# Optimization experiments

Measured on AMD Instinct MI355X. Metric: run time of the kernel, lower is better.

## Reference

```python
import jax, jax.numpy as jnp
import numpy as np

B, L, D, H = 2, 4096, 768, 12
HS = D // H  # head_size = 64
SCALE = HS ** -0.5


def setup_inputs() -> dict:
    key = jax.random.key(0)
    k1, k2, k3 = jax.random.split(key, 3)
    x = jax.random.normal(k1, (B, L, D), dtype=jnp.float32)
    # torch nn.Linear weights are [out_features, in_features]; y = x @ W.T
    Wq = jax.random.normal(k2, (D, D), dtype=jnp.float32) * (D ** -0.5)
    Wo = jax.random.normal(k3, (D, D), dtype=jnp.float32) * (D ** -0.5)
    return {"x": x, "Wq": Wq, "Wo": Wo}


def reference(x, Wq, Wo):
    b, l, d = x.shape
    # NOTE: source module uses self.query for Q, K, AND V (bug preserved).
    q = jnp.einsum('bld,ed->ble', x, Wq)              # [B,L,D]
    q = q.reshape(b, l, H, HS).transpose(0, 2, 1, 3)   # [B,H,L,HS]
    k = v = q                                          # K = V = Q (faithful)
    scores = jnp.einsum('bhqd,bhkd->bhqk', q, k) * SCALE  # [B,H,L,L]
    attn = jax.nn.softmax(scores, axis=-1)
    out = jnp.einsum('bhqk,bhkd->bhqd', attn, v)       # [B,H,L,HS]
    out = out.transpose(0, 2, 1, 3).reshape(b, l, d)   # [B,L,D]
    out = jnp.einsum('bld,ed->ble', out, Wo)           # output projection
    return out
```

## Files before the change

### kernel.cpp

```cpp
#include <hip/hip_runtime.h>
#include <hip/hip_bf16.h>

#define LQ 4096
#define DQ 768
#define NH 12
#define NB 2

typedef __attribute__((ext_vector_type(8))) short short8;
typedef __attribute__((ext_vector_type(2))) unsigned uint2v;
typedef __attribute__((ext_vector_type(4))) float f32x4;

__device__ __forceinline__ short f2bf(float f) {
    union { float f; unsigned u; } v; v.f = f;
    unsigned r = v.u + 0x7FFFu + ((v.u >> 16) & 1u);
    return (short)(r >> 16);
}

__device__ __forceinline__ unsigned pk2(float a, float b) {
    float2 t; t.x = a; t.y = b;
    __hip_bfloat162 h = __float22bfloat162_rn(t);
    unsigned u; __builtin_memcpy(&u, &h, 4);
    return u;
}

__device__ __forceinline__ f32x4 mfma16(short8 a, short8 b, f32x4 c) {
    return __builtin_amdgcn_mfma_f32_16x16x32_bf16(a, b, c, 0, 0, 0);
}

__device__ __forceinline__ void gld16(const short* g, short* l) {
    __builtin_amdgcn_global_load_lds(
        (const __attribute__((address_space(1))) unsigned int*)(g),
        (__attribute__((address_space(3))) unsigned int*)(l), 16, 0, 0);
}

#define SQRT_C 0.424660891f

__global__ __launch_bounds__(256) void cvtw(const float* __restrict__ a,
                                            short* __restrict__ o) {
    int i = blockIdx.x * 256 + threadIdx.x;
    float4 v = ((const float4*)a)[i];
    *(uint2v*)&o[i * 4] = (uint2v){pk2(v.x, v.y), pk2(v.z, v.w)};
}


template <int MODE>
__global__ __launch_bounds__(256, 3) void gemm_nt(const short* __restrict__ A,
                                                  const short* __restrict__ Wb,
                                                  void* __restrict__ Cp,
                                                  short* __restrict__ Vf) {
    __shared__ __attribute__((aligned(16))) short As[2][128 * 64];
    __shared__ __attribute__((aligned(16))) short Bs[2][64 * 64];
    const int t = threadIdx.x;
    const int lane = t & 63, w = t >> 6;
    const int lr = lane & 15, qd = lane >> 4;
    const int wm = (w & 1) * 64, wn = (w >> 1) * 32;
    const int lin = blockIdx.x;
    const int xcd = lin & 7, jj = lin >> 3;
    const int nt = jj % 12, mt = (jj / 12) * 8 + xcd;
    const int m0 = mt * 128, n0 = nt * 64;

    int aoffs[4], boffs[2];
#pragma unroll
    for (int u = 0; u < 4; ++u) {
        int c = (u * 4 + w) * 64 + lane;
        int row = c >> 3, k = (c & 7) ^ (row & 7);
        aoffs[u] = (m0 + row) * DQ + k * 8;
    }
#pragma unroll
    for (int u = 0; u < 2; ++u) {
        int c = (u * 4 + w) * 64 + lane;
        int row = c >> 3, k = (c & 7) ^ (row & 7);
        boffs[u] = (n0 + row) * DQ + k * 8;
    }

    f32x4 acc[4][2];
#pragma unroll
    for (int i = 0; i < 4; ++i)
#pragma unroll
        for (int j = 0; j < 2; ++j) acc[i][j] = (f32x4){0.f, 0.f, 0.f, 0.f};

#pragma unroll
    for (int u = 0; u < 4; ++u) gld16(&A[aoffs[u]], &As[0][(u * 4 + w) * 512]);
#pragma unroll
    for (int u = 0; u < 2; ++u) gld16(&Wb[boffs[u]], &Bs[0][(u * 4 + w) * 512]);
    __syncthreads();

    int cur = 0;
    for (int kt = 0; kt < 12; ++kt) {
        if (kt < 11) {
            const int k0 = (kt + 1) * 64;
#pragma unroll
            for (int u = 0; u < 4; ++u) gld16(&A[aoffs[u] + k0], &As[cur ^ 1][(u * 4 + w) * 512]);
#pragma unroll
            for (int u = 0; u < 2; ++u) gld16(&Wb[boffs[u] + k0], &Bs[cur ^ 1][(u * 4 + w) * 512]);
        }
#pragma unroll
        for (int s = 0; s < 2; ++s) {
            const int cq = ((4 * s + qd) ^ (lr & 7)) * 8;
            short8 af[4], bf[2];
#pragma unroll
            for (int i = 0; i < 4; ++i)
                af[i] = *(short8*)&As[cur][(wm + 16 * i + lr) * 64 + cq];
#pragma unroll
            for (int j = 0; j < 2; ++j)
                bf[j] = *(short8*)&Bs[cur][(wn + 16 * j + lr) * 64 + cq];
#pragma unroll
            for (int i = 0; i < 4; ++i)
#pragma unroll
                for (int j = 0; j < 2; ++j)
                    acc[i][j] = mfma16(af[i], bf[j], acc[i][j]);
        }
        __syncthreads();
        cur ^= 1;
    }

    if (MODE == 0) {
#pragma unroll
        for (int i = 0; i < 4; ++i)
#pragma unroll
            for (int j = 0; j < 2; ++j) {
                const int row0 = m0 + wm + 16 * i + qd * 4;
                const int col = n0 + wn + 16 * j + lr;
#pragma unroll
                for (int r = 0; r < 4; ++r)
                    ((float*)Cp)[(size_t)(row0 + r) * DQ + col] = acc[i][j][r];
            }
    } else {
        short* Qf = (short*)Cp;
        short* F = (short*)As;
        const int bh = (m0 >> 12) * NH + nt;
        const size_t gbase = (size_t)bh * (LQ * 64) + (size_t)(((m0 & 4095) >> 6) << 12);
#pragma unroll
        for (int i = 0; i < 4; ++i)
#pragma unroll
            for (int j = 0; j < 2; ++j) {
                const int kl = wm + 16 * i + qd * 4;
                const int hs = wn + 16 * j + lr;
                const int fi = ((kl >> 6) << 12) + ((((hs >> 4) << 1) + ((kl >> 5) & 1)) << 9)
                             + (((hs & 15) + (((kl >> 3) & 3) << 4)) << 3) + (kl & 7);
                *(uint2v*)&F[fi] = (uint2v){pk2(acc[i][j][0], acc[i][j][1]),
                                            pk2(acc[i][j][2], acc[i][j][3])};
            }
        __syncthreads();
#pragma unroll
        for (int p = 0; p < 4; ++p) {
            int u = t + 256 * p;
            *(short8*)&Vf[gbase + (size_t)u * 8] = *(short8*)&F[u * 8];
        }
        __syncthreads();
#pragma unroll
        for (int i = 0; i < 4; ++i)
#pragma unroll
            for (int j = 0; j < 2; ++j) {
                const int hs = wn + 16 * j + lr;
#pragma unroll
                for (int r = 0; r < 4; ++r) {
                    const int key = wm + 16 * i + qd * 4 + r;
                    const int fi = ((key >> 6) << 12) + (((((key >> 4) & 3) << 1) + (hs >> 5)) << 9)
                                 + (((qd * 4 + r) + (((hs >> 3) & 3) << 4)) << 3) + (hs & 7);
                    F[fi] = f2bf(acc[i][j][r] * SQRT_C);
                }
            }
        __syncthreads();
#pragma unroll
        for (int p = 0; p < 4; ++p) {
            int u = t + 256 * p;
            *(short8*)&Qf[gbase + (size_t)u * 8] = *(short8*)&F[u * 8];
        }
    }
}

__global__ __launch_bounds__(256, 3) void attn(const short* __restrict__ Qf,
                                               const short* __restrict__ Vf,
                                               short* __restrict__ O) {
    const int linear = blockIdx.x;
    const int xcd = linear & 7, slot = linear >> 3;
    const int bh = 3 * xcd + (slot >> 5);
    const int qtile = slot & 31;
    const int t = threadIdx.x;
    const int lane = t & 63, w = t >> 6;
    const int qw = w & 1, half = w >> 1;
    const int lr = lane & 15, qd = lane >> 4;

    __shared__ alignas(16) char smem[43008];
    short* aqs = (short*)smem;
    short* Ps = (short*)(smem + 16384) + w * 2560;

    const short* Qbh = Qf + (size_t)bh * (LQ * 64);
    const short* Vbh = Vf + (size_t)bh * (LQ * 64);
    const int q0 = qtile * 128 + qw * 64;
    const int kb0 = half * 64;

    const short one_bf = (short)0x3F80;
    short8 ones;
#pragma unroll
    for (int j = 0; j < 8; ++j) ones[j] = one_bf;

#pragma unroll
    for (int p = 0; p < 4; ++p) {
        int off = (t + 256 * p) * 8;
        *(short8*)&aqs[off] = *(const short8*)&Qbh[(size_t)qtile * 8192 + off];
    }
    __syncthreads();

    f32x4 oacc[4][4], lacc[4];
#pragma unroll
    for (int i = 0; i < 4; ++i) {
        lacc[i] = (f32x4){0.f, 0.f, 0.f, 0.f};
#pragma unroll
        for (int t2 = 0; t2 < 4; ++t2) oacc[i][t2] = (f32x4){0.f, 0.f, 0.f, 0.f};
    }

    const int aqbase = qw * 4096 + lane * 8;

    for (int kb = kb0; kb < kb0 + 64; ++kb) {
        short8 kf[2][2];
#pragma unroll
        for (int t4 = 0; t4 < 2; ++t4)
#pragma unroll
            for (int s = 0; s < 2; ++s)
                kf[t4][s] = *(const short8*)&Qbh[kb * 2048 + (t4 * 2 + s) * 512 + lane * 8];

#pragma unroll
        for (int i = 0; i < 4; ++i) {
            short8 aq0 = *(const short8*)&aqs[aqbase + i * 1024];
            short8 aq1 = *(const short8*)&aqs[aqbase + i * 1024 + 512];
            f32x4 s0 = (f32x4){0.f, 0.f, 0.f, 0.f};
            f32x4 s1 = (f32x4){0.f, 0.f, 0.f, 0.f};
            s0 = mfma16(kf[0][0], aq0, s0);
            s0 = mfma16(kf[0][1], aq1, s0);
            s1 = mfma16(kf[1][0], aq0, s1);
            s1 = mfma16(kf[1][1], aq1, s1);
            *(uint2v*)&Ps[i * 640 + lr * 40 + 4 * qd] =
                (uint2v){pk2(__builtin_amdgcn_exp2f(s0[0]), __builtin_amdgcn_exp2f(s0[1])),
                         pk2(__builtin_amdgcn_exp2f(s0[2]), __builtin_amdgcn_exp2f(s0[3]))};
            *(uint2v*)&Ps[i * 640 + lr * 40 + 16 + 4 * qd] =
                (uint2v){pk2(__builtin_amdgcn_exp2f(s1[0]), __builtin_amdgcn_exp2f(s1[1])),
                         pk2(__builtin_amdgcn_exp2f(s1[2]), __builtin_amdgcn_exp2f(s1[3]))};
        }

        short8 vb[4];
#pragma unroll
        for (int t2 = 0; t2 < 4; ++t2)
            vb[t2] = *(const short8*)&Vbh[(kb >> 1) * 4096 + (kb & 1) * 512 + t2 * 1024 + lane * 8];

#pragma unroll
        for (int i = 0; i < 4; ++i) {
            short8 pa = *(short8*)&Ps[i * 640 + lr * 40 + qd * 8];
#pragma unroll
            for (int t2 = 0; t2 < 4; ++t2)
                oacc[i][t2] = mfma16(pa, vb[t2], oacc[i][t2]);
            lacc[i] = mfma16(pa, ones, lacc[i]);
        }
    }

    __syncthreads();
    f32x4* ex = (f32x4*)smem + (qw * 64 + lane) * 21;
    if (half) {
#pragma unroll
        for (int i = 0; i < 4; ++i) {
#pragma unroll
            for (int t2 = 0; t2 < 4; ++t2) ex[i * 4 + t2] = oacc[i][t2];
            ex[16 + i] = lacc[i];
        }
    }
    __syncthreads();
    if (half) return;

#pragma unroll
    for (int i = 0; i < 4; ++i) {
#pragma unroll
        for (int t2 = 0; t2 < 4; ++t2) oacc[i][t2] += ex[i * 4 + t2];
        lacc[i] += ex[16 + i];
    }

    const int b = bh / NH, h = bh % NH;
#pragma unroll
    for (int i = 0; i < 4; ++i) {
        float inv[4];
#pragma unroll
        for (int r = 0; r < 4; ++r) inv[r] = 1.0f / lacc[i][r];
#pragma unroll
        for (int t2 = 0; t2 < 4; ++t2)
#pragma unroll
            for (int r = 0; r < 4; ++r) {
                int lq = q0 + 16 * i + qd * 4 + r;
                int e = h * 64 + 16 * t2 + lr;
                O[((size_t)(b * LQ + lq)) * DQ + e] = f2bf(oacc[i][t2][r] * inv[r]);
            }
    }
}

extern "C" void kernel_launch(void* const* d_in, const int* in_sizes, int n_in,
                              void* d_out, int out_size, void* d_ws, size_t ws_size,
                              hipStream_t stream) {
    (void)in_sizes; (void)n_in; (void)out_size; (void)ws_size;
    const float* x  = (const float*)d_in[0];
    const float* Wq = (const float*)d_in[1];
    const float* Wo = (const float*)d_in[2];
    float* out = (float*)d_out;

    const size_t NQ = (size_t)NB * NH * LQ * 64;
    const size_t NW = (size_t)DQ * DQ;
    short* Qf  = (short*)d_ws;
    short* Vfb = Qf + NQ;
    short* Ows = Vfb + NQ;
    short* Wqb = Ows + (size_t)NB * LQ * DQ;
    short* Wob = Wqb + NW;

    cvtw<<<(NB * LQ * DQ) / 1024, 256, 0, stream>>>(x, Ows);
    cvtw<<<NW / 1024, 256, 0, stream>>>(Wq, Wqb);
    cvtw<<<NW / 1024, 256, 0, stream>>>(Wo, Wob);
    gemm_nt<1><<<768, 256, 0, stream>>>(Ows, Wqb, Qf, Vfb);
    attn<<<768, 256, 0, stream>>>(Qf, Vfb, Ows);
    gemm_nt<0><<<768, 256, 0, stream>>>(Ows, Wob, out, nullptr);
}
```

Baseline: 233.4 us.

## Load GEMM fragments directly from global memory and raise priority around attention MFMAs

The projection GEMM drops its double-buffered LDS staging through global_load_lds and instead reads MFMA operand fragments straight from global memory into registers each k-step. This removes the LDS round trip and the per-iteration barriers, at the cost of less coalesced, uncached-reuse global loads and no prefetch overlap. Separately, the attention loop wraps its MFMA groups in s_setprio(1)/s_setprio(0) so waves issuing matrix ops are favoured by the scheduler over waves doing exp and LDS work.

```diff
diff --git a/kernel.cpp b/kernel.cpp
--- a/kernel.cpp
+++ b/kernel.cpp
@@ -27,12 +27,6 @@
     return __builtin_amdgcn_mfma_f32_16x16x32_bf16(a, b, c, 0, 0, 0);
 }
 
-__device__ __forceinline__ void gld16(const short* g, short* l) {
-    __builtin_amdgcn_global_load_lds(
-        (const __attribute__((address_space(1))) unsigned int*)(g),
-        (__attribute__((address_space(3))) unsigned int*)(l), 16, 0, 0);
-}
-
 #define SQRT_C 0.424660891f
 
 __global__ __launch_bounds__(256) void cvtw(const float* __restrict__ a,
@@ -48,8 +42,7 @@
                                                   const short* __restrict__ Wb,
                                                   void* __restrict__ Cp,
                                                   short* __restrict__ Vf) {
-    __shared__ __attribute__((aligned(16))) short As[2][128 * 64];
-    __shared__ __attribute__((aligned(16))) short Bs[2][64 * 64];
+    __shared__ __attribute__((aligned(16))) short F[8192];
     const int t = threadIdx.x;
     const int lane = t & 63, w = t >> 6;
     const int lr = lane & 15, qd = lane >> 4;
@@ -59,19 +52,14 @@
     const int nt = jj % 12, mt = (jj / 12) * 8 + xcd;
     const int m0 = mt * 128, n0 = nt * 64;
 
-    int aoffs[4], boffs[2];
-#pragma unroll
-    for (int u = 0; u < 4; ++u) {
-        int c = (u * 4 + w) * 64 + lane;
-        int row = c >> 3, k = (c & 7) ^ (row & 7);
-        aoffs[u] = (m0 + row) * DQ + k * 8;
-    }
-#pragma unroll
-    for (int u = 0; u < 2; ++u) {
-        int c = (u * 4 + w) * 64 + lane;
-        int row = c >> 3, k = (c & 7) ^ (row & 7);
-        boffs[u] = (n0 + row) * DQ + k * 8;
-    }
+    const short* ap[4];
+    const short* bp[2];
+#pragma unroll
+    for (int i = 0; i < 4; ++i)
+        ap[i] = A + (size_t)(m0 + wm + 16 * i + lr) * DQ + qd * 8;
+#pragma unroll
+    for (int j = 0; j < 2; ++j)
+        bp[j] = Wb + (size_t)(n0 + wn + 16 * j + lr) * DQ + qd * 8;
 
     f32x4 acc[4][2];
 #pragma unroll
@@ -79,39 +67,25 @@
 #pragma unroll
         for (int j = 0; j < 2; ++j) acc[i][j] = (f32x4){0.f, 0.f, 0.f, 0.f};
 
-#pragma unroll
-    for (int u = 0; u < 4; ++u) gld16(&A[aoffs[u]], &As[0][(u * 4 + w) * 512]);
-#pragma unroll
-    for (int u = 0; u < 2; ++u) gld16(&Wb[boffs[u]], &Bs[0][(u * 4 + w) * 512]);
-    __syncthreads();
-
-    int cur = 0;
     for (int kt = 0; kt < 12; ++kt) {
-        if (kt < 11) {
-            const int k0 = (kt + 1) * 64;
-#pragma unroll
-            for (int u = 0; u < 4; ++u) gld16(&A[aoffs[u] + k0], &As[cur ^ 1][(u * 4 + w) * 512]);
-#pragma unroll
-            for (int u = 0; u < 2; ++u) gld16(&Wb[boffs[u] + k0], &Bs[cur ^ 1][(u * 4 + w) * 512]);
-        }
-#pragma unroll
-        for (int s = 0; s < 2; ++s) {
-            const int cq = ((4 * s + qd) ^ (lr & 7)) * 8;
-            short8 af[4], bf[2];
+        short8 af[4][2], bf[2][2];
+#pragma unroll
+        for (int i = 0; i < 4; ++i)
+#pragma unroll
+            for (int s = 0; s < 2; ++s)
+                af[i][s] = *(const short8*)&ap[i][kt * 64 + s * 32];
+#pragma unroll
+        for (int j = 0; j < 2; ++j)
+#pragma unroll
+            for (int s = 0; s < 2; ++s)
+                bf[j][s] = *(const short8*)&bp[j][kt * 64 + s * 32];
+#pragma unroll
+        for (int s = 0; s < 2; ++s)
 #pragma unroll
             for (int i = 0; i < 4; ++i)
-                af[i] = *(short8*)&As[cur][(wm + 16 * i + lr) * 64 + cq];
-#pragma unroll
-            for (int j = 0; j < 2; ++j)
-                bf[j] = *(short8*)&Bs[cur][(wn + 16 * j + lr) * 64 + cq];
-#pragma unroll
-            for (int i = 0; i < 4; ++i)
 #pragma unroll
                 for (int j = 0; j < 2; ++j)
-                    acc[i][j] = mfma16(af[i], bf[j], acc[i][j]);
-        }
-        __syncthreads();
-        cur ^= 1;
+                    acc[i][j] = mfma16(af[i][s], bf[j][s], acc[i][j]);
     }
 
     if (MODE == 0) {
@@ -127,7 +101,6 @@
             }
     } else {
         short* Qf = (short*)Cp;
-        short* F = (short*)As;
         const int bh = (m0 >> 12) * NH + nt;
         const size_t gbase = (size_t)bh * (LQ * 64) + (size_t)(((m0 & 4095) >> 6) << 12);
 #pragma unroll
@@ -227,10 +200,12 @@
             short8 aq1 = *(const short8*)&aqs[aqbase + i * 1024 + 512];
             f32x4 s0 = (f32x4){0.f, 0.f, 0.f, 0.f};
             f32x4 s1 = (f32x4){0.f, 0.f, 0.f, 0.f};
+            __builtin_amdgcn_s_setprio(1);
             s0 = mfma16(kf[0][0], aq0, s0);
             s0 = mfma16(kf[0][1], aq1, s0);
             s1 = mfma16(kf[1][0], aq0, s1);
             s1 = mfma16(kf[1][1], aq1, s1);
+            __builtin_amdgcn_s_setprio(0);
             *(uint2v*)&Ps[i * 640 + lr * 40 + 4 * qd] =
                 (uint2v){pk2(__builtin_amdgcn_exp2f(s0[0]), __builtin_amdgcn_exp2f(s0[1])),
                          pk2(__builtin_amdgcn_exp2f(s0[2]), __builtin_amdgcn_exp2f(s0[3]))};
@@ -244,6 +219,7 @@
         for (int t2 = 0; t2 < 4; ++t2)
             vb[t2] = *(const short8*)&Vbh[(kb >> 1) * 4096 + (kb & 1) * 512 + t2 * 1024 + lane * 8];
 
+        __builtin_amdgcn_s_setprio(1);
 #pragma unroll
         for (int i = 0; i < 4; ++i) {
             short8 pa = *(short8*)&Ps[i * 640 + lr * 40 + qd * 8];
@@ -252,6 +228,7 @@
                 oacc[i][t2] = mfma16(pa, vb[t2], oacc[i][t2]);
             lacc[i] = mfma16(pa, ones, lacc[i]);
         }
+        __builtin_amdgcn_s_setprio(0);
     }
 
     __syncthreads();
```

Result: slower. 300.0 us (+28.5%).
